# Performance work log

Measured on AMD Instinct MI355X. Metric: run time of the kernel, lower is better.

Reference implementation:

```python
import jax, jax.numpy as jnp
import numpy as np
import math

HEADS = 16
D_MODEL = 1024
HEAD_DIM = D_MODEL // HEADS
B, S = 2, 2048


def setup_inputs() -> dict:
    key = jax.random.key(0)
    ks = jax.random.split(key, 12)
    sc = 1.0 / math.sqrt(D_MODEL)
    inp = {
        "query": jax.random.normal(ks[0], (B, S, D_MODEL), jnp.float32),
        "key_t": jax.random.normal(ks[1], (B, S, D_MODEL), jnp.float32),
        "value": jax.random.normal(ks[2], (B, S, D_MODEL), jnp.float32),
        "mask": jax.random.randint(ks[3], (B, 1, 1, S), 0, 2, jnp.int32),
        "Wq": jax.random.normal(ks[4], (D_MODEL, D_MODEL), jnp.float32) * sc,
        "bq": jnp.zeros((D_MODEL,), jnp.float32),
        "Wk": jax.random.normal(ks[5], (D_MODEL, D_MODEL), jnp.float32) * sc,
        "bk": jnp.zeros((D_MODEL,), jnp.float32),
        "Wv": jax.random.normal(ks[6], (D_MODEL, D_MODEL), jnp.float32) * sc,
        "bv": jnp.zeros((D_MODEL,), jnp.float32),
        "Wo": jax.random.normal(ks[7], (D_MODEL, D_MODEL), jnp.float32) * sc,
        "bo": jnp.zeros((D_MODEL,), jnp.float32),
    }
    return inp


def _split_heads(x):
    # [B, S, D] -> [B, H, S, Dh]
    b, s, _ = x.shape
    return x.reshape(b, s, HEADS, HEAD_DIM).transpose(0, 2, 1, 3)


def reference(query, key_t, value, mask, Wq, bq, Wk, bk, Wv, bv, Wo, bo):
    # Linear projections (torch Linear: x @ W.T + b)
    q = _split_heads(query @ Wq.T + bq)
    k = _split_heads(key_t @ Wk.T + bk)
    v = _split_heads(value @ Wv.T + bv)
    # Scaled dot-product attention; scale by sqrt(head_dim) = query.size(-1) after split
    scores = jnp.einsum("bhqd,bhkd->bhqk", q, k) / math.sqrt(HEAD_DIM)
    scores = jnp.where(mask == 0, jnp.float32(-1e9), scores)
    prob = jax.nn.softmax(scores, axis=-1)
    # dropout is identity at inference
    attn = jnp.einsum("bhqk,bhkd->bhqd", prob, v)
    # [B, H, S, Dh] -> [B, S, D]
    attn = attn.transpose(0, 2, 1, 3).reshape(query.shape[0], -1, D_MODEL)
    return attn @ Wo.T + bo
```

## Files before the change

kernel.cpp:

```cpp
#include <hip/hip_runtime.h>
#include <hip/hip_bf16.h>

typedef __bf16 bf16;
typedef __bf16 bf16x8 __attribute__((ext_vector_type(8)));
typedef __bf16 bf16x4 __attribute__((ext_vector_type(4)));
typedef float  f32x4  __attribute__((ext_vector_type(4)));
typedef float  f32x16 __attribute__((ext_vector_type(16)));

#define AS1 __attribute__((address_space(1)))
#define AS3 __attribute__((address_space(3)))

__device__ __forceinline__ void gload_lds16(const bf16* g, bf16* l) {
    __builtin_amdgcn_global_load_lds((const AS1 unsigned int*)g,
                                     (AS3 unsigned int*)l, 16, 0, 0);
}

__global__ __launch_bounds__(256) void cast7_k(
    const float* __restrict__ s0, const float* __restrict__ s1,
    const float* __restrict__ s2, const float* __restrict__ s3,
    const float* __restrict__ s4, const float* __restrict__ s5,
    const float* __restrict__ s6,
    bf16* __restrict__ d0, bf16* __restrict__ d1, bf16* __restrict__ d2,
    bf16* __restrict__ d3, bf16* __restrict__ d4, bf16* __restrict__ d5,
    bf16* __restrict__ d6, int n_big, int n_small) {
    int z = blockIdx.z;
    const float* s = (z == 0) ? s0 : (z == 1) ? s1 : (z == 2) ? s2
                   : (z == 3) ? s3 : (z == 4) ? s4 : (z == 5) ? s5 : s6;
    bf16* d = (z == 0) ? d0 : (z == 1) ? d1 : (z == 2) ? d2
            : (z == 3) ? d3 : (z == 4) ? d4 : (z == 5) ? d5 : d6;
    int n = (z < 3) ? n_big : n_small;
    int i = (blockIdx.x * 256 + threadIdx.x) * 8;
    if (i >= n) return;
    float4 a = *(const float4*)(s + i);
    float4 b = *(const float4*)(s + i + 4);
    bf16x8 o;
    o[0] = (bf16)a.x; o[1] = (bf16)a.y; o[2] = (bf16)a.z; o[3] = (bf16)a.w;
    o[4] = (bf16)b.x; o[5] = (bf16)b.y; o[6] = (bf16)b.z; o[7] = (bf16)b.w;
    *(bf16x8*)(d + i) = o;
}

__global__ __launch_bounds__(256) void mask_bias_k(
    const int* __restrict__ m, float* __restrict__ mb, int n) {
    int i = blockIdx.x * 256 + threadIdx.x;
    if (i < n) mb[i] = (m[i] == 0) ? -1.442695e9f : -17.3123405f;
}

template <typename OUT_T, bool TRANS, int MT>
__device__ __forceinline__ void gemm32_core(
    const bf16* __restrict__ A, const bf16* __restrict__ W,
    const float* __restrict__ bias, OUT_T* __restrict__ C,
    int M, int N, int K) {
    constexpr int MI = MT / 64;
    __shared__ bf16 Asm[MT * 64];
    __shared__ bf16 Bsm[128 * 64];
    const int lane = threadIdx.x & 63;
    const int w = threadIdx.x >> 6;
    const int l31 = lane & 31;
    const int h = lane >> 5;
    const int x7 = l31 & 7;
    const int m0 = blockIdx.x * MT;
    const int n0 = blockIdx.y * 128;
    const int srow = lane >> 3;
    const int scol = ((lane & 7) ^ srow) * 8;
    const int wm = (w & 1) * (MT / 2);
    const int wn = (w >> 1) * 64;

    f32x16 acc[MI][2] = {};

    for (int k0 = 0; k0 < K; k0 += 64) {
#pragma unroll
        for (int c = 0; c < MT / 32; ++c) {
            int r = w * (MT / 4) + c * 8;
            gload_lds16(A + (size_t)(m0 + r + srow) * K + k0 + scol, &Asm[r * 64]);
        }
#pragma unroll
        for (int c = 0; c < 4; ++c) {
            int r = w * 32 + c * 8;
            gload_lds16(W + (size_t)(n0 + r + srow) * K + k0 + scol, &Bsm[r * 64]);
        }
        __syncthreads();
#pragma unroll
        for (int step = 0; step < 4; ++step) {
            bf16x8 af[MI], bfv[2];
#pragma unroll
            for (int i = 0; i < MI; ++i)
                af[i] = *(const bf16x8*)&Asm[(wm + i * 32 + l31) * 64 +
                                             (((step * 2 + h) ^ x7) * 8)];
#pragma unroll
            for (int j = 0; j < 2; ++j)
                bfv[j] = *(const bf16x8*)&Bsm[(wn + j * 32 + l31) * 64 +
                                              (((step * 2 + h) ^ x7) * 8)];
#pragma unroll
            for (int i = 0; i < MI; ++i)
#pragma unroll
                for (int j = 0; j < 2; ++j)
                    acc[i][j] = TRANS
                        ? __builtin_amdgcn_mfma_f32_32x32x16_bf16(bfv[j], af[i],
                                                                  acc[i][j], 0, 0, 0)
                        : __builtin_amdgcn_mfma_f32_32x32x16_bf16(af[i], bfv[j],
                                                                  acc[i][j], 0, 0, 0);
        }
        __syncthreads();
    }
    if (!TRANS) {
#pragma unroll
        for (int i = 0; i < MI; ++i)
#pragma unroll
            for (int j = 0; j < 2; ++j) {
                int col = n0 + wn + j * 32 + l31;
                float bv = bias[col];
#pragma unroll
                for (int g = 0; g < 4; ++g)
#pragma unroll
                    for (int rr = 0; rr < 4; ++rr) {
                        int row = m0 + wm + i * 32 + rr + g * 8 + 4 * h;
                        C[(size_t)row * N + col] =
                            (OUT_T)(acc[i][j][g * 4 + rr] + bv);
                    }
            }
    } else {
#pragma unroll
        for (int i = 0; i < MI; ++i) {
            int s = m0 + wm + i * 32 + l31;
            int b = s >> 11;
            int sl = s & 2047;
            int sp = (sl & ~12) | ((sl & 4) << 1) | ((sl & 8) >> 1);
#pragma unroll
            for (int j = 0; j < 2; ++j)
#pragma unroll
                for (int g = 0; g < 4; ++g) {
                    float4 bv4 = *(const float4*)&bias[n0 + wn + j * 32 + g * 8 + 4 * h];
#pragma unroll
                    for (int rr = 0; rr < 4; ++rr) {
                        int n = n0 + wn + j * 32 + g * 8 + 4 * h + rr;
                        C[(size_t)(b * 1024 + n) * 2048 + sp] =
                            (OUT_T)(acc[i][j][g * 4 + rr] + (&bv4.x)[rr]);
                    }
                }
        }
    }
}

__global__ __launch_bounds__(256) void gemm_qkv(
    const bf16* __restrict__ qb, const bf16* __restrict__ kb, const bf16* __restrict__ vb,
    const bf16* __restrict__ Wq, const bf16* __restrict__ Wk, const bf16* __restrict__ Wv,
    const float* __restrict__ bq, const float* __restrict__ bk, const float* __restrict__ bv,
    bf16* __restrict__ Qp, bf16* __restrict__ Kp, bf16* __restrict__ VpT) {
    int z = blockIdx.z;
    if (z == 2) {
        gemm32_core<bf16, true, 128>(vb, Wv, bv, VpT, 4096, 1024, 1024);
    } else {
        const bf16* A = (z == 0) ? qb : kb;
        const bf16* W = (z == 0) ? Wq : Wk;
        const float* bi = (z == 0) ? bq : bk;
        bf16* C = (z == 0) ? Qp : Kp;
        gemm32_core<bf16, false, 128>(A, W, bi, C, 4096, 1024, 1024);
    }
}

__global__ __launch_bounds__(256) void gemm_out(
    const bf16* __restrict__ A, const bf16* __restrict__ W,
    const float* __restrict__ bias, float* __restrict__ C) {
    gemm32_core<float, false, 64>(A, W, bias, C, 4096, 1024, 1024);
}

__global__ __launch_bounds__(256, 2) void attn_k(
    const bf16* __restrict__ Qp, const bf16* __restrict__ Kp,
    const bf16* __restrict__ VpT, const float* __restrict__ mb,
    bf16* __restrict__ Opart, float* __restrict__ Lpart) {
    __shared__ bf16 KV[2][2][64 * 64];
    const int qb = blockIdx.x;
    const int bh = blockIdx.y;
    const int sp = blockIdx.z;
    const int b = bh >> 4, hh = bh & 15;
    const int lane = threadIdx.x & 63, w = threadIdx.x >> 6;
    const int l31 = lane & 31, h = lane >> 5;
    const int x7 = l31 & 7;
    const int srow = lane >> 3, scol = ((lane & 7) ^ srow) * 8;
    const float SC = 0.125f * 1.44269504f;
    const int q0 = qb * 256;
    const int k0 = sp * 512;

    const bf16* Kg = Kp + (size_t)(b * 2048) * 1024 + hh * 64;
    const bf16* Vg = VpT + (size_t)bh * 64 * 2048;
    const float* mbb = mb + b * 2048;

    auto stage = [&](int buf, int kt) {
#pragma unroll
        for (int c = 0; c < 2; ++c) {
            int r = w * 16 + c * 8;
            gload_lds16(Kg + (size_t)(kt + r + srow) * 1024 + scol,
                        &KV[buf][0][r * 64]);
            gload_lds16(Vg + (size_t)(r + srow) * 2048 + kt + scol,
                        &KV[buf][1][r * 64]);
        }
    };
    stage(0, k0);

    bf16x8 qf[2][4];
#pragma unroll
    for (int qg = 0; qg < 2; ++qg) {
        const bf16* Qbase =
            Qp + (size_t)(b * 2048 + q0 + w * 64 + qg * 32 + l31) * 1024 + hh * 64;
#pragma unroll
        for (int step = 0; step < 4; ++step)
            qf[qg][step] = *(const bf16x8*)(Qbase + step * 16 + h * 8);
    }

    f32x16 o[2][2] = {};
    float lsum[2] = {0.0f, 0.0f};

    for (int it = 0; it < 8; ++it) {
        __syncthreads();
        if (it < 7) stage((it + 1) & 1, k0 + (it + 1) * 64);
        const bf16* Ks = KV[it & 1][0];
        const bf16* Vs = KV[it & 1][1];
        const int kt = k0 + it * 64;

        bf16x8 pa[2][4];
#pragma unroll
        for (int kg = 0; kg < 2; ++kg) {
            f32x16 z0 = {}, z1 = {};
#pragma unroll
            for (int step = 0; step < 4; ++step) {
                bf16x8 kf = *(const bf16x8*)&Ks[(kg * 32 + l31) * 64 +
                                                (((step * 2 + h) ^ x7) * 8)];
                z0 = __builtin_amdgcn_mfma_f32_32x32x16_bf16(kf, qf[0][step], z0, 0, 0, 0);
                z1 = __builtin_amdgcn_mfma_f32_32x32x16_bf16(kf, qf[1][step], z1, 0, 0, 0);
            }
#pragma unroll
            for (int g = 0; g < 4; ++g) {
                float4 bia = *(const float4*)&mbb[kt + kg * 32 + g * 8 + 4 * h];
#pragma unroll
                for (int qg = 0; qg < 2; ++qg) {
                    const f32x16& z = qg ? z1 : z0;
                    float p0 = __builtin_amdgcn_exp2f(fmaf(z[g * 4 + 0], SC, bia.x));
                    float p1 = __builtin_amdgcn_exp2f(fmaf(z[g * 4 + 1], SC, bia.y));
                    float p2 = __builtin_amdgcn_exp2f(fmaf(z[g * 4 + 2], SC, bia.z));
                    float p3 = __builtin_amdgcn_exp2f(fmaf(z[g * 4 + 3], SC, bia.w));
                    lsum[qg] += (p0 + p1) + (p2 + p3);
                    bf16x8& pf = pa[qg][kg * 2 + (g >> 1)];
                    int jb = (g & 1) * 4;
                    pf[jb + 0] = (bf16)p0;
                    pf[jb + 1] = (bf16)p1;
                    pf[jb + 2] = (bf16)p2;
                    pf[jb + 3] = (bf16)p3;
                }
            }
        }
#pragma unroll
        for (int t = 0; t < 2; ++t)
#pragma unroll
            for (int kk = 0; kk < 4; ++kk) {
                bf16x8 vf = *(const bf16x8*)&Vs[(t * 32 + l31) * 64 +
                                                (((kk * 2 + h) ^ x7) * 8)];
                o[0][t] = __builtin_amdgcn_mfma_f32_32x32x16_bf16(pa[0][kk], vf, o[0][t], 0, 0, 0);
                o[1][t] = __builtin_amdgcn_mfma_f32_32x32x16_bf16(pa[1][kk], vf, o[1][t], 0, 0, 0);
            }
    }

    const size_t pbase = (size_t)(sp * 32 + bh) * 2048;
#pragma unroll
    for (int qg = 0; qg < 2; ++qg) {
        float ls = lsum[qg] + __shfl_xor(lsum[qg], 32, 64);
        if (h == 0)
            Lpart[pbase + q0 + w * 64 + qg * 32 + l31] = ls;
#pragma unroll
        for (int t = 0; t < 2; ++t)
#pragma unroll
            for (int g = 0; g < 4; ++g)
#pragma unroll
                for (int rr = 0; rr < 4; ++rr) {
                    int q = q0 + w * 64 + qg * 32 + rr + g * 8 + 4 * h;
                    Opart[(pbase + q) * 64 + t * 32 + l31] =
                        (bf16)o[qg][t][g * 4 + rr];
                }
    }
}

__global__ __launch_bounds__(256) void combine_k(
    const bf16* __restrict__ Op, const float* __restrict__ Lp,
    bf16* __restrict__ Ao) {
    int idx = blockIdx.x * 256 + threadIdx.x;
    int d8 = idx & 7;
    int q = (idx >> 3) & 2047;
    int bh = idx >> 14;
    float acc[8] = {};
    float l = 0.0f;
#pragma unroll
    for (int sp = 0; sp < 4; ++sp) {
        size_t base = (size_t)(sp * 32 + bh) * 2048 + q;
        bf16x8 v = *(const bf16x8*)&Op[base * 64 + d8 * 8];
        l += Lp[base];
#pragma unroll
        for (int i = 0; i < 8; ++i) acc[i] += (float)v[i];
    }
    float inv = 1.0f / l;
    bf16x8 ov;
#pragma unroll
    for (int i = 0; i < 8; ++i) ov[i] = (bf16)(acc[i] * inv);
    int b = bh >> 4, hh = bh & 15;
    *(bf16x8*)&Ao[(size_t)(b * 2048 + q) * 1024 + hh * 64 + d8 * 8] = ov;
}

extern "C" void kernel_launch(void* const* d_in, const int* in_sizes, int n_in,
                              void* d_out, int out_size, void* d_ws, size_t ws_size,
                              hipStream_t stream) {
    const float* q   = (const float*)d_in[0];
    const float* kt  = (const float*)d_in[1];
    const float* v   = (const float*)d_in[2];
    const int* mask  = (const int*)d_in[3];
    const float* Wq  = (const float*)d_in[4];
    const float* bq  = (const float*)d_in[5];
    const float* Wk  = (const float*)d_in[6];
    const float* bk  = (const float*)d_in[7];
    const float* Wv  = (const float*)d_in[8];
    const float* bv  = (const float*)d_in[9];
    const float* Wo  = (const float*)d_in[10];
    const float* bo  = (const float*)d_in[11];
    float* out = (float*)d_out;

    char* ws = (char*)d_ws;
    const size_t SZ_IN = 4096ull * 1024 * 2;
    const size_t SZ_W  = 1024ull * 1024 * 2;
    bf16* qb  = (bf16*)(ws + 0 * SZ_IN);
    bf16* kb  = (bf16*)(ws + 1 * SZ_IN);
    bf16* vb  = (bf16*)(ws + 2 * SZ_IN);
    bf16* Wqb = (bf16*)(ws + 3 * SZ_IN);
    bf16* Wkb = (bf16*)(ws + 3 * SZ_IN + 1 * SZ_W);
    bf16* Wvb = (bf16*)(ws + 3 * SZ_IN + 2 * SZ_W);
    bf16* Wob = (bf16*)(ws + 3 * SZ_IN + 3 * SZ_W);
    bf16* Qp  = (bf16*)(ws + 3 * SZ_IN + 4 * SZ_W);
    bf16* Kp  = (bf16*)(ws + 4 * SZ_IN + 4 * SZ_W);
    bf16* VpT = (bf16*)(ws + 5 * SZ_IN + 4 * SZ_W);
    float* mb = (float*)(ws + 6 * SZ_IN + 4 * SZ_W);
    char*  p0 = ws + 6 * SZ_IN + 4 * SZ_W + (1 << 20);
    bf16* Opart = (bf16*)p0;
    float* Lpart = (float*)(p0 + 4ull * 32 * 2048 * 64 * 2);
    bf16* Ao  = qb;

    const int NIN = 4096 * 1024, NW = 1024 * 1024;
    cast7_k<<<dim3(NIN / 2048, 1, 7), 256, 0, stream>>>(
        q, kt, v, Wq, Wk, Wv, Wo, qb, kb, vb, Wqb, Wkb, Wvb, Wob, NIN, NW);
    mask_bias_k<<<16, 256, 0, stream>>>(mask, mb, 4096);

    gemm_qkv<<<dim3(32, 8, 3), 256, 0, stream>>>(qb, kb, vb, Wqb, Wkb, Wvb,
                                                 bq, bk, bv, Qp, Kp, VpT);
    attn_k<<<dim3(8, 32, 4), 256, 0, stream>>>(Qp, Kp, VpT, mb, Opart, Lpart);
    combine_k<<<2048, 256, 0, stream>>>(Opart, Lpart, Ao);
    gemm_out<<<dim3(64, 8), 256, 0, stream>>>(Ao, Wob, bo, out);
}
```

Baseline: 228.5 us.

## Fuse split-K combine into output GEMM, halve attention splits, merge mask kernel into cast

Attention now splits the key range in 2 instead of 4 and uses a flattened 1D grid. The separate combine kernel is removed: the output projection GEMM reads the two partial outputs and row sums, normalizes them, and writes the A tile to LDS itself. The mask-bias kernel is folded into the cast kernel as an extra z slice. Together these remove two launches and the Ao round-trip through memory. The cost is less attention parallelism (512 blocks instead of 1024) and redundant combine work repeated across each N tile of the output GEMM.

```diff
diff --git a/kernel.cpp b/kernel.cpp
--- a/kernel.cpp
+++ b/kernel.cpp
@@ -15,21 +15,40 @@
                                      (AS3 unsigned int*)l, 16, 0, 0);
 }
 
-__global__ __launch_bounds__(256) void cast7_k(
+__global__ __launch_bounds__(256) void cast8_k(
     const float* __restrict__ s0, const float* __restrict__ s1,
     const float* __restrict__ s2, const float* __restrict__ s3,
     const float* __restrict__ s4, const float* __restrict__ s5,
     const float* __restrict__ s6,
     bf16* __restrict__ d0, bf16* __restrict__ d1, bf16* __restrict__ d2,
     bf16* __restrict__ d3, bf16* __restrict__ d4, bf16* __restrict__ d5,
-    bf16* __restrict__ d6, int n_big, int n_small) {
+    bf16* __restrict__ d6,
+    const int* __restrict__ m, float* __restrict__ mb,
+    int n_big, int n_small) {
     int z = blockIdx.z;
+    int i = (blockIdx.x * 256 + threadIdx.x) * 8;
+    if (z == 7) {
+        if (i >= 4096) return;
+        int4 a = *(const int4*)(m + i);
+        int4 b = *(const int4*)(m + i + 4);
+        float4 o0, o1;
+        o0.x = (a.x == 0) ? -1.442695e9f : -17.3123405f;
+        o0.y = (a.y == 0) ? -1.442695e9f : -17.3123405f;
+        o0.z = (a.z == 0) ? -1.442695e9f : -17.3123405f;
+        o0.w = (a.w == 0) ? -1.442695e9f : -17.3123405f;
+        o1.x = (b.x == 0) ? -1.442695e9f : -17.3123405f;
+        o1.y = (b.y == 0) ? -1.442695e9f : -17.3123405f;
+        o1.z = (b.z == 0) ? -1.442695e9f : -17.3123405f;
+        o1.w = (b.w == 0) ? -1.442695e9f : -17.3123405f;
+        *(float4*)(mb + i) = o0;
+        *(float4*)(mb + i + 4) = o1;
+        return;
+    }
     const float* s = (z == 0) ? s0 : (z == 1) ? s1 : (z == 2) ? s2
                    : (z == 3) ? s3 : (z == 4) ? s4 : (z == 5) ? s5 : s6;
     bf16* d = (z == 0) ? d0 : (z == 1) ? d1 : (z == 2) ? d2
             : (z == 3) ? d3 : (z == 4) ? d4 : (z == 5) ? d5 : d6;
     int n = (z < 3) ? n_big : n_small;
-    int i = (blockIdx.x * 256 + threadIdx.x) * 8;
     if (i >= n) return;
     float4 a = *(const float4*)(s + i);
     float4 b = *(const float4*)(s + i + 4);
@@ -39,51 +58,40 @@
     *(bf16x8*)(d + i) = o;
 }
 
-__global__ __launch_bounds__(256) void mask_bias_k(
-    const int* __restrict__ m, float* __restrict__ mb, int n) {
-    int i = blockIdx.x * 256 + threadIdx.x;
-    if (i < n) mb[i] = (m[i] == 0) ? -1.442695e9f : -17.3123405f;
-}
-
-template <typename OUT_T, bool TRANS, int MT>
+template <typename OUT_T, bool TRANS>
 __device__ __forceinline__ void gemm32_core(
     const bf16* __restrict__ A, const bf16* __restrict__ W,
     const float* __restrict__ bias, OUT_T* __restrict__ C,
     int M, int N, int K) {
-    constexpr int MI = MT / 64;
-    __shared__ bf16 Asm[MT * 64];
+    __shared__ bf16 Asm[128 * 64];
     __shared__ bf16 Bsm[128 * 64];
     const int lane = threadIdx.x & 63;
     const int w = threadIdx.x >> 6;
     const int l31 = lane & 31;
     const int h = lane >> 5;
     const int x7 = l31 & 7;
-    const int m0 = blockIdx.x * MT;
+    const int m0 = blockIdx.x * 128;
     const int n0 = blockIdx.y * 128;
     const int srow = lane >> 3;
     const int scol = ((lane & 7) ^ srow) * 8;
-    const int wm = (w & 1) * (MT / 2);
+    const int wm = (w & 1) * 64;
     const int wn = (w >> 1) * 64;
 
-    f32x16 acc[MI][2] = {};
+    f32x16 acc[2][2] = {};
 
     for (int k0 = 0; k0 < K; k0 += 64) {
-#pragma unroll
-        for (int c = 0; c < MT / 32; ++c) {
-            int r = w * (MT / 4) + c * 8;
-            gload_lds16(A + (size_t)(m0 + r + srow) * K + k0 + scol, &Asm[r * 64]);
-        }
 #pragma unroll
         for (int c = 0; c < 4; ++c) {
             int r = w * 32 + c * 8;
+            gload_lds16(A + (size_t)(m0 + r + srow) * K + k0 + scol, &Asm[r * 64]);
             gload_lds16(W + (size_t)(n0 + r + srow) * K + k0 + scol, &Bsm[r * 64]);
         }
         __syncthreads();
 #pragma unroll
         for (int step = 0; step < 4; ++step) {
-            bf16x8 af[MI], bfv[2];
-#pragma unroll
-            for (int i = 0; i < MI; ++i)
+            bf16x8 af[2], bfv[2];
+#pragma unroll
+            for (int i = 0; i < 2; ++i)
                 af[i] = *(const bf16x8*)&Asm[(wm + i * 32 + l31) * 64 +
                                              (((step * 2 + h) ^ x7) * 8)];
 #pragma unroll
@@ -91,7 +99,7 @@
                 bfv[j] = *(const bf16x8*)&Bsm[(wn + j * 32 + l31) * 64 +
                                               (((step * 2 + h) ^ x7) * 8)];
 #pragma unroll
-            for (int i = 0; i < MI; ++i)
+            for (int i = 0; i < 2; ++i)
 #pragma unroll
                 for (int j = 0; j < 2; ++j)
                     acc[i][j] = TRANS
@@ -104,7 +112,7 @@
     }
     if (!TRANS) {
 #pragma unroll
-        for (int i = 0; i < MI; ++i)
+        for (int i = 0; i < 2; ++i)
 #pragma unroll
             for (int j = 0; j < 2; ++j) {
                 int col = n0 + wn + j * 32 + l31;
@@ -120,7 +128,7 @@
             }
     } else {
 #pragma unroll
-        for (int i = 0; i < MI; ++i) {
+        for (int i = 0; i < 2; ++i) {
             int s = m0 + wm + i * 32 + l31;
             int b = s >> 11;
             int sl = s & 2047;
@@ -148,20 +156,90 @@
     bf16* __restrict__ Qp, bf16* __restrict__ Kp, bf16* __restrict__ VpT) {
     int z = blockIdx.z;
     if (z == 2) {
-        gemm32_core<bf16, true, 128>(vb, Wv, bv, VpT, 4096, 1024, 1024);
+        gemm32_core<bf16, true>(vb, Wv, bv, VpT, 4096, 1024, 1024);
     } else {
         const bf16* A = (z == 0) ? qb : kb;
         const bf16* W = (z == 0) ? Wq : Wk;
         const float* bi = (z == 0) ? bq : bk;
         bf16* C = (z == 0) ? Qp : Kp;
-        gemm32_core<bf16, false, 128>(A, W, bi, C, 4096, 1024, 1024);
-    }
-}
-
-__global__ __launch_bounds__(256) void gemm_out(
-    const bf16* __restrict__ A, const bf16* __restrict__ W,
-    const float* __restrict__ bias, float* __restrict__ C) {
-    gemm32_core<float, false, 64>(A, W, bias, C, 4096, 1024, 1024);
+        gemm32_core<bf16, false>(A, W, bi, C, 4096, 1024, 1024);
+    }
+}
+
+__global__ __launch_bounds__(256) void gemm_out_fused(
+    const bf16* __restrict__ Op, const float* __restrict__ Lp,
+    const bf16* __restrict__ W, const float* __restrict__ bias,
+    float* __restrict__ C) {
+    __shared__ bf16 Asm[64 * 64];
+    __shared__ bf16 Bsm[128 * 64];
+    const int id = blockIdx.x;
+    const int m0 = (id & 63) * 64;
+    const int n0 = (id >> 6) * 128;
+    const int lane = threadIdx.x & 63;
+    const int w = threadIdx.x >> 6;
+    const int l31 = lane & 31;
+    const int h = lane >> 5;
+    const int x7 = l31 & 7;
+    const int srow = lane >> 3;
+    const int l7 = lane & 7;
+    const int scol = (l7 ^ srow) * 8;
+    const int wm = (w & 1) * 32;
+    const int wn = (w >> 1) * 64;
+
+    f32x16 acc[2] = {};
+
+    for (int k0 = 0; k0 < 1024; k0 += 64) {
+#pragma unroll
+        for (int c = 0; c < 2; ++c) {
+            int r = w * 16 + c * 8;
+            int row = m0 + r + srow;
+            int colb = k0 + scol;
+            int b = row >> 11, q = row & 2047;
+            int hh = colb >> 6, d = colb & 63;
+            size_t l0i = (size_t)(b * 16 + hh) * 2048 + q;
+            bf16x8 v0 = *(const bf16x8*)&Op[l0i * 64 + d];
+            bf16x8 v1 = *(const bf16x8*)&Op[(l0i + 32 * 2048) * 64 + d];
+            float inv = 1.0f / (Lp[l0i] + Lp[l0i + 32 * 2048]);
+            bf16x8 o;
+#pragma unroll
+            for (int i = 0; i < 8; ++i)
+                o[i] = (bf16)(((float)v0[i] + (float)v1[i]) * inv);
+            *(bf16x8*)&Asm[(r + srow) * 64 + l7 * 8] = o;
+        }
+#pragma unroll
+        for (int c = 0; c < 4; ++c) {
+            int r = w * 32 + c * 8;
+            gload_lds16(W + (size_t)(n0 + r + srow) * 1024 + k0 + scol, &Bsm[r * 64]);
+        }
+        __syncthreads();
+#pragma unroll
+        for (int step = 0; step < 4; ++step) {
+            bf16x8 af = *(const bf16x8*)&Asm[(wm + l31) * 64 +
+                                             (((step * 2 + h) ^ x7) * 8)];
+            bf16x8 bfv[2];
+#pragma unroll
+            for (int j = 0; j < 2; ++j)
+                bfv[j] = *(const bf16x8*)&Bsm[(wn + j * 32 + l31) * 64 +
+                                              (((step * 2 + h) ^ x7) * 8)];
+#pragma unroll
+            for (int j = 0; j < 2; ++j)
+                acc[j] = __builtin_amdgcn_mfma_f32_32x32x16_bf16(af, bfv[j],
+                                                                 acc[j], 0, 0, 0);
+        }
+        __syncthreads();
+    }
+#pragma unroll
+    for (int j = 0; j < 2; ++j) {
+        int col = n0 + wn + j * 32 + l31;
+        float bv = bias[col];
+#pragma unroll
+        for (int g = 0; g < 4; ++g)
+#pragma unroll
+            for (int rr = 0; rr < 4; ++rr) {
+                int row = m0 + wm + rr + g * 8 + 4 * h;
+                C[(size_t)row * 1024 + col] = acc[j][g * 4 + rr] + bv;
+            }
+    }
 }
 
 __global__ __launch_bounds__(256, 2) void attn_k(
@@ -169,9 +247,10 @@
     const bf16* __restrict__ VpT, const float* __restrict__ mb,
     bf16* __restrict__ Opart, float* __restrict__ Lpart) {
     __shared__ bf16 KV[2][2][64 * 64];
-    const int qb = blockIdx.x;
-    const int bh = blockIdx.y;
-    const int sp = blockIdx.z;
+    const int g = blockIdx.x;
+    const int qb = g >> 6;
+    const int bh = (g & 63) >> 1;
+    const int sp = g & 1;
     const int b = bh >> 4, hh = bh & 15;
     const int lane = threadIdx.x & 63, w = threadIdx.x >> 6;
     const int l31 = lane & 31, h = lane >> 5;
@@ -179,7 +258,7 @@
     const int srow = lane >> 3, scol = ((lane & 7) ^ srow) * 8;
     const float SC = 0.125f * 1.44269504f;
     const int q0 = qb * 256;
-    const int k0 = sp * 512;
+    const int k0 = sp * 1024;
 
     const bf16* Kg = Kp + (size_t)(b * 2048) * 1024 + hh * 64;
     const bf16* Vg = VpT + (size_t)bh * 64 * 2048;
@@ -210,9 +289,9 @@
     f32x16 o[2][2] = {};
     float lsum[2] = {0.0f, 0.0f};
 
-    for (int it = 0; it < 8; ++it) {
+    for (int it = 0; it < 16; ++it) {
         __syncthreads();
-        if (it < 7) stage((it + 1) & 1, k0 + (it + 1) * 64);
+        if (it < 15) stage((it + 1) & 1, k0 + (it + 1) * 64);
         const bf16* Ks = KV[it & 1][0];
         const bf16* Vs = KV[it & 1][1];
         const int kt = k0 + it * 64;
@@ -276,31 +355,6 @@
                         (bf16)o[qg][t][g * 4 + rr];
                 }
     }
-}
-
-__global__ __launch_bounds__(256) void combine_k(
-    const bf16* __restrict__ Op, const float* __restrict__ Lp,
-    bf16* __restrict__ Ao) {
-    int idx = blockIdx.x * 256 + threadIdx.x;
-    int d8 = idx & 7;
-    int q = (idx >> 3) & 2047;
-    int bh = idx >> 14;
-    float acc[8] = {};
-    float l = 0.0f;
-#pragma unroll
-    for (int sp = 0; sp < 4; ++sp) {
-        size_t base = (size_t)(sp * 32 + bh) * 2048 + q;
-        bf16x8 v = *(const bf16x8*)&Op[base * 64 + d8 * 8];
-        l += Lp[base];
-#pragma unroll
-        for (int i = 0; i < 8; ++i) acc[i] += (float)v[i];
-    }
-    float inv = 1.0f / l;
-    bf16x8 ov;
-#pragma unroll
-    for (int i = 0; i < 8; ++i) ov[i] = (bf16)(acc[i] * inv);
-    int b = bh >> 4, hh = bh & 15;
-    *(bf16x8*)&Ao[(size_t)(b * 2048 + q) * 1024 + hh * 64 + d8 * 8] = ov;
 }
 
 extern "C" void kernel_launch(void* const* d_in, const int* in_sizes, int n_in,
@@ -336,17 +390,15 @@
     float* mb = (float*)(ws + 6 * SZ_IN + 4 * SZ_W);
     char*  p0 = ws + 6 * SZ_IN + 4 * SZ_W + (1 << 20);
     bf16* Opart = (bf16*)p0;
-    float* Lpart = (float*)(p0 + 4ull * 32 * 2048 * 64 * 2);
-    bf16* Ao  = qb;
+    float* Lpart = (float*)(p0 + 2ull * 32 * 2048 * 64 * 2);
 
     const int NIN = 4096 * 1024, NW = 1024 * 1024;
-    cast7_k<<<dim3(NIN / 2048, 1, 7), 256, 0, stream>>>(
-        q, kt, v, Wq, Wk, Wv, Wo, qb, kb, vb, Wqb, Wkb, Wvb, Wob, NIN, NW);
-    mask_bias_k<<<16, 256, 0, stream>>>(mask, mb, 4096);
+    cast8_k<<<dim3(NIN / 2048, 1, 8), 256, 0, stream>>>(
+        q, kt, v, Wq, Wk, Wv, Wo, qb, kb, vb, Wqb, Wkb, Wvb, Wob,
+        mask, mb, NIN, NW);
 
     gemm_qkv<<<dim3(32, 8, 3), 256, 0, stream>>>(qb, kb, vb, Wqb, Wkb, Wvb,
                                                  bq, bk, bv, Qp, Kp, VpT);
-    attn_k<<<dim3(8, 32, 4), 256, 0, stream>>>(Qp, Kp, VpT, mb, Opart, Lpart);
-    combine_k<<<2048, 256, 0, stream>>>(Opart, Lpart, Ao);
-    gemm_out<<<dim3(64, 8), 256, 0, stream>>>(Ao, Wob, bo, out);
-}
+    attn_k<<<dim3(512), 256, 0, stream>>>(Qp, Kp, VpT, mb, Opart, Lpart);
+    gemm_out_fused<<<dim3(512), 256, 0, stream>>>(Opart, Lpart, Wob, bo, out);
+}
```

New measurement: 225.3 us. Within noise of the previous version (-1.4%).
